# Kernel tuning notes

Measured on AMD Instinct MI355X. Metric: run time of the kernel, lower is better.

Reference implementation:

```python
import jax, jax.numpy as jnp
import numpy as np

NUM_HEADS = 16
BLOCK_SIZE = 64
NUM_GLOBAL_TOKENS = 64
WINDOW_SIZE = 256
NUM_RANDOM_BLOCKS = 3
BATCH = 2
SEQ_LEN = 4096
EMBED_DIM = 1024


def _alibi_slopes(n):
    # power-of-2 head count path of _compute_alibi_slopes
    base = 2.0 ** (-(2.0 ** (-(np.log2(n) - 3.0))))
    return jnp.asarray([base ** i for i in range(1, n + 1)], dtype=jnp.float32)


def _build_block_indices():
    nb = SEQ_LEN // BLOCK_SIZE
    ngb = NUM_GLOBAL_TOKENS // BLOCK_SIZE
    wb = WINDOW_SIZE // BLOCK_SIZE
    mb = 2 * wb + 1 + NUM_RANDOM_BLOCKS
    rng = np.random.default_rng(0)
    out = np.full((nb, mb), -1, dtype=np.int64)
    for qb in range(nb):
        attended = set(range(ngb))  # global blocks handled separately
        idx = 0
        for kb in range(max(ngb, qb - wb), min(nb, qb + wb + 1)):
            if kb not in attended:
                out[qb, idx] = kb
                attended.add(kb)
                idx += 1
        cand = [b for b in range(ngb, nb) if b not in attended]
        pick = rng.choice(len(cand), size=min(NUM_RANDOM_BLOCKS, len(cand)), replace=False)
        for j in pick:
            out[qb, idx] = cand[j]
            idx += 1
    return jnp.asarray(out)


def setup_inputs() -> dict:
    key = jax.random.key(0)
    ks = jax.random.split(key, 5)
    s = 0.02
    x = jax.random.normal(ks[0], (BATCH, SEQ_LEN, EMBED_DIM), jnp.float32)
    Wq = jax.random.normal(ks[1], (EMBED_DIM, EMBED_DIM), jnp.float32) * s
    Wk = jax.random.normal(ks[2], (EMBED_DIM, EMBED_DIM), jnp.float32) * s
    Wv = jax.random.normal(ks[3], (EMBED_DIM, EMBED_DIM), jnp.float32) * s
    Wo = jax.random.normal(ks[4], (EMBED_DIM, EMBED_DIM), jnp.float32) * s
    return {"x": x, "Wq": Wq, "Wk": Wk, "Wv": Wv, "Wo": Wo,
            "block_indices": _build_block_indices()}


def reference(x, Wq, Wk, Wv, Wo, block_indices):
    B, S, E = x.shape
    H = NUM_HEADS
    Dh = E // H
    G = NUM_GLOBAL_TOKENS
    BS = BLOCK_SIZE
    scale = 1.0 / np.sqrt(Dh)

    def split_heads(t):
        return t.reshape(B, S, H, Dh).transpose(0, 2, 1, 3)  # [B,H,S,Dh]

    q = split_heads(x @ Wq)
    k = split_heads(x @ Wk)
    v = split_heads(x @ Wv)

    slopes = _alibi_slopes(H)  # [H]
    pos = jnp.arange(S, dtype=jnp.float32)

    # ---- global tokens: full attention over all keys ----
    sg = jnp.einsum('bhgd,bhsd->bhgs', q[:, :, :G], k) * scale
    bias_g = -slopes[:, None, None] * jnp.abs(pos[:G, None] - pos[None, :])  # [H,G,S]
    pg = jax.nn.softmax(sg + bias_g[None], axis=-1)
    out_g = jnp.einsum('bhgs,bhsd->bhgd', pg, v)  # [B,H,G,Dh]

    # ---- sparse queries: global KV + gathered sparse blocks ----
    nb = S // BS
    ngb = G // BS
    nqb = nb - ngb
    bi = block_indices[ngb:]           # [nqb, MB], -1 = padding
    mb = bi.shape[1]
    bsafe = jnp.maximum(bi, 0)

    kb = k.reshape(B, H, nb, BS, Dh)
    vb = v.reshape(B, H, nb, BS, Dh)
    kg = kb[:, :, bsafe].reshape(B, H, nqb, mb * BS, Dh)
    vg = vb[:, :, bsafe].reshape(B, H, nqb, mb * BS, Dh)
    kglob = jnp.broadcast_to(k[:, :, None, :G], (B, H, nqb, G, Dh))
    vglob = jnp.broadcast_to(v[:, :, None, :G], (B, H, nqb, G, Dh))
    kcat = jnp.concatenate([kglob, kg], axis=3)  # [B,H,nqb,G+mb*BS,Dh]
    vcat = jnp.concatenate([vglob, vg], axis=3)

    qn = q[:, :, G:].reshape(B, H, nqb, BS, Dh)
    scores = jnp.einsum('bhqmd,bhqnd->bhqmn', qn, kcat) * scale

    qpos = (G + jnp.arange(nqb * BS, dtype=jnp.float32)).reshape(nqb, BS)
    loc_pos = (bsafe[:, :, None] * BS + jnp.arange(BS)[None, None, :]).reshape(nqb, mb * BS).astype(jnp.float32)
    kpos = jnp.concatenate([jnp.broadcast_to(pos[:G][None], (nqb, G)), loc_pos], axis=1)
    bias = -slopes[:, None, None, None] * jnp.abs(qpos[None, :, :, None] - kpos[None, :, None, :])  # [H,nqb,BS,Kt]

    valid = jnp.concatenate([jnp.ones((nqb, G), bool), jnp.repeat(bi >= 0, BS, axis=1)], axis=1)
    scores = jnp.where(valid[None, None, :, None, :], scores + bias[None], -jnp.inf)
    p = jax.nn.softmax(scores, axis=-1)
    out_s = jnp.einsum('bhqmn,bhqnd->bhqmd', p, vcat).reshape(B, H, S - G, Dh)

    out = jnp.concatenate([out_g, out_s], axis=2)  # [B,H,S,Dh]
    out = out.transpose(0, 2, 1, 3).reshape(B, S, E)
    return out @ Wo
```

## Files before the change

kernel.cpp:

```cpp
#include <hip/hip_runtime.h>
#include <stdint.h>

typedef __attribute__((ext_vector_type(8))) short short8;
typedef __attribute__((ext_vector_type(4))) float f32x4;
typedef __attribute__((ext_vector_type(8))) unsigned short u16x8;

#define DEV static __device__ __forceinline__

DEV unsigned short f2bf(float f) {
  union { float f; uint32_t u; } v; v.f = f;
  uint32_t r = v.u + 0x7FFFu + ((v.u >> 16) & 1u);
  return (unsigned short)(r >> 16);
}

DEV void gload16(const void* g, void* l) {
  __builtin_amdgcn_global_load_lds(
      (const __attribute__((address_space(1))) void*)g,
      (__attribute__((address_space(3))) void*)l, 16, 0, 0);
}

__global__ void cast_x_kernel(const float* __restrict__ x, unsigned short* __restrict__ xb) {
  int i = blockIdx.x * 256 + threadIdx.x;
  f32x4 a = ((const f32x4*)x)[2 * i];
  f32x4 b = ((const f32x4*)x)[2 * i + 1];
  u16x8 o;
  o[0] = f2bf(a[0]); o[1] = f2bf(a[1]); o[2] = f2bf(a[2]); o[3] = f2bf(a[3]);
  o[4] = f2bf(b[0]); o[5] = f2bf(b[1]); o[6] = f2bf(b[2]); o[7] = f2bf(b[3]);
  ((u16x8*)xb)[i] = o;
}

__global__ void transpose_w_kernel(const float* __restrict__ Wq, const float* __restrict__ Wk,
                                   const float* __restrict__ Wv, const float* __restrict__ Wo,
                                   unsigned short* __restrict__ wt) {
  __shared__ float tile[64][65];
  int z = blockIdx.z;
  const float* W = (z == 0) ? Wq : (z == 1) ? Wk : (z == 2) ? Wv : Wo;
  unsigned short* dst = wt + (size_t)z * 1024 * 1024;
  int bn = blockIdx.x, bk = blockIdx.y;
  int t = threadIdx.x;
  int c = t & 63, rr = t >> 6;
#pragma unroll
  for (int p = 0; p < 16; ++p) {
    int r = p * 4 + rr;
    tile[r][c] = W[(size_t)(bk * 64 + r) * 1024 + bn * 64 + c];
  }
  __syncthreads();
#pragma unroll
  for (int p = 0; p < 16; ++p) {
    int r2 = p * 4 + rr;
    dst[(size_t)(bn * 64 + r2) * 1024 + bk * 64 + c] = f2bf(tile[c][r2]);
  }
}

template <int MODE>
__global__ __launch_bounds__(256, 2) void gemm_bt(const unsigned short* __restrict__ A,
                                                  const unsigned short* __restrict__ Bt,
                                                  void* __restrict__ dst, float escale) {
  constexpr int K = 1024;
  __shared__ __align__(16) unsigned short As[128 * 64];
  __shared__ __align__(16) unsigned short Bs[128 * 64];
  int bn = blockIdx.x, bm = blockIdx.y;
  int tid = threadIdx.x, lane = tid & 63, w = tid >> 6;
  int wr = w >> 1, wc = w & 1;
  f32x4 acc[4][4] = {};

  int sr[4], soff[4];
#pragma unroll
  for (int i = 0; i < 4; ++i) {
    int ci = w * 4 + i;
    int r = ci * 8 + (lane >> 3);
    int cc = lane & 7;
    int scc = cc ^ (r & 7);
    sr[i] = r;
    soff[i] = scc * 8;
  }
  const unsigned short* Arow = A + (size_t)(bm * 128) * K;
  const unsigned short* Brow = Bt + (size_t)(bn * 128) * K;

  for (int k0 = 0; k0 < K; k0 += 64) {
#pragma unroll
    for (int i = 0; i < 4; ++i) {
      gload16(Arow + (size_t)sr[i] * K + k0 + soff[i], As + (w * 4 + i) * 512);
      gload16(Brow + (size_t)sr[i] * K + k0 + soff[i], Bs + (w * 4 + i) * 512);
    }
    __syncthreads();
    short8 af[2][4], bfr[2][4];
#pragma unroll
    for (int c = 0; c < 2; ++c) {
#pragma unroll
      for (int m = 0; m < 4; ++m) {
        int cc = (lane >> 4) + 4 * c;
        int ra = wr * 64 + m * 16 + (lane & 15);
        af[c][m] = *(const short8*)(As + ra * 64 + ((cc ^ (ra & 7)) * 8));
        int rb = wc * 64 + m * 16 + (lane & 15);
        bfr[c][m] = *(const short8*)(Bs + rb * 64 + ((cc ^ (rb & 7)) * 8));
      }
    }
#pragma unroll
    for (int c = 0; c < 2; ++c)
#pragma unroll
      for (int m = 0; m < 4; ++m)
#pragma unroll
        for (int n = 0; n < 4; ++n)
          acc[m][n] = __builtin_amdgcn_mfma_f32_16x16x32_bf16(af[c][m], bfr[c][n], acc[m][n], 0, 0, 0);
    __syncthreads();
  }

  int rbase = bm * 128 + wr * 64;
  int cbase = bn * 128 + wc * 64;
#pragma unroll
  for (int m = 0; m < 4; ++m)
#pragma unroll
    for (int n = 0; n < 4; ++n) {
      int row0 = rbase + m * 16 + (lane >> 4) * 4;
      int col = cbase + n * 16 + (lane & 15);
#pragma unroll
      for (int reg = 0; reg < 4; ++reg) {
        int row = row0 + reg;
        float v = acc[m][n][reg] * escale;
        if (MODE == 0) {
          ((float*)dst)[(size_t)row * 1024 + col] = v;
        } else {
          int b = row >> 12, s = row & 4095;
          int h = col >> 6, d = col & 63;
          if (MODE == 1)
            ((unsigned short*)dst)[((size_t)(b * 16 + h) * 4096 + s) * 64 + d] = f2bf(v);
          else
            ((unsigned short*)dst)[(((size_t)(b * 16 + h) * 64 + (s >> 6)) * 64 + d) * 64 + (s & 63)] = f2bf(v);
        }
      }
    }
}

__global__ __launch_bounds__(256) void attn_kernel(const unsigned short* __restrict__ Qh,
                            const unsigned short* __restrict__ Kh,
                            const unsigned short* __restrict__ Vbt,
                            const int* __restrict__ bidx,
                            unsigned short* __restrict__ attn_out,
                            float* __restrict__ Opart,
                            float* __restrict__ lpart) {
  __shared__ __align__(16) unsigned short Ks[2][64 * 64];
  __shared__ __align__(16) unsigned short Vs[2][64 * 64];
  __shared__ __align__(16) unsigned short Pl[4][16][72];
  int flat = blockIdx.x + 71 * blockIdx.y;
  int nf = (flat & 7) * 284 + (flat >> 3);
  int gx = nf % 71, bh = nf / 71;
  int h = bh & 15;
  int tid = threadIdx.x, lane = tid & 63, w = tid >> 6;
  float slope2 = exp2f(-0.5f * (float)(h + 1)) * 1.44269504f;

  int qb, nkb;
  int list[13];
  if (gx < 63) {
    qb = gx + 1;
    nkb = 1;
    list[0] = 0;
#pragma unroll
    for (int j = 0; j < 12; ++j) {
      int v = bidx[qb * 12 + j];
      if (v >= 0) list[nkb++] = v;
    }
  } else {
    qb = 0;
    int chunk = gx - 63;
    nkb = 8;
#pragma unroll
    for (int i = 0; i < 8; ++i) list[i] = chunk * 8 + i;
  }

  int qrow = qb * 64 + w * 16 + (lane & 15);
  const unsigned short* qptr = Qh + ((size_t)bh * 4096 + qrow) * 64 + (lane >> 4) * 8;
  short8 qf0 = *(const short8*)qptr;
  short8 qf1 = *(const short8*)(qptr + 32);

  float psum[4] = {0.f, 0.f, 0.f, 0.f};
  f32x4 accO[4] = {};
  int qpos0 = qb * 64 + w * 16 + (lane >> 4) * 4;

  const unsigned short* Kbh = Kh + (size_t)bh * 4096 * 64;
  const unsigned short* Vbh = Vbt + (size_t)bh * 4096 * 64;

  int sr[2], so[2];
#pragma unroll
  for (int i = 0; i < 2; ++i) {
    int ci = w * 2 + i;
    int r = ci * 8 + (lane >> 3);
    sr[i] = r;
    so[i] = ((lane & 7) ^ (r & 7)) * 8;
  }
  auto STAGE = [&](int bi, int kb) {
    const unsigned short* kbase = Kbh + (size_t)kb * 4096;
    const unsigned short* vbase = Vbh + (size_t)kb * 4096;
#pragma unroll
    for (int i = 0; i < 2; ++i) {
      gload16(kbase + sr[i] * 64 + so[i], &Ks[bi][(w * 2 + i) * 512]);
      gload16(vbase + sr[i] * 64 + so[i], &Vs[bi][(w * 2 + i) * 512]);
    }
  };

  STAGE(0, list[0]);

  for (int it = 0; it < nkb; ++it) {
    int cur = it & 1;
    int kb = list[it];
    __syncthreads();
    if (it + 1 < nkb) STAGE(cur ^ 1, list[it + 1]);

    float pv[4][4];
#pragma unroll
    for (int ct = 0; ct < 4; ++ct) {
      int kr = ct * 16 + (lane & 15);
      short8 kf0 = *(const short8*)(&Ks[cur][kr * 64 + (((lane >> 4) ^ (kr & 7)) * 8)]);
      short8 kf1 = *(const short8*)(&Ks[cur][kr * 64 + ((((lane >> 4) + 4) ^ (kr & 7)) * 8)]);
      f32x4 s = __builtin_amdgcn_mfma_f32_16x16x32_bf16(qf0, kf0, (f32x4){0.f, 0.f, 0.f, 0.f}, 0, 0, 0);
      s = __builtin_amdgcn_mfma_f32_16x16x32_bf16(qf1, kf1, s, 0, 0, 0);
      int kpos = kb * 64 + ct * 16 + (lane & 15);
#pragma unroll
      for (int reg = 0; reg < 4; ++reg) {
        float dp = fabsf((float)(qpos0 + reg - kpos));
        float p = exp2f(__builtin_fmaf(-slope2, dp, s[reg]));
        pv[ct][reg] = p;
        psum[reg] += p;
      }
    }
#pragma unroll
    for (int cp = 0; cp < 2; ++cp)
#pragma unroll
      for (int reg = 0; reg < 4; ++reg) {
        uint32_t pk;
        asm("v_cvt_pk_bf16_f32 %0, %1, %2" : "=v"(pk) : "v"(pv[2 * cp][reg]), "v"(pv[2 * cp + 1][reg]));
        int row = (lane >> 4) * 4 + reg;
        int c = lane & 15;
        Pl[w][row][cp * 32 + c] = (unsigned short)pk;
        Pl[w][row][cp * 32 + 16 + c] = (unsigned short)(pk >> 16);
      }

    asm volatile("s_waitcnt lgkmcnt(0)" ::: "memory");
    short8 pa0 = *(const short8*)(&Pl[w][lane & 15][(lane >> 4) * 8]);
    short8 pa1 = *(const short8*)(&Pl[w][lane & 15][(lane >> 4) * 8 + 32]);
#pragma unroll
    for (int dt = 0; dt < 4; ++dt) {
      int dr = dt * 16 + (lane & 15);
      short8 vf0 = *(const short8*)(&Vs[cur][dr * 64 + (((lane >> 4) ^ (dr & 7)) * 8)]);
      short8 vf1 = *(const short8*)(&Vs[cur][dr * 64 + ((((lane >> 4) + 4) ^ (dr & 7)) * 8)]);
      accO[dt] = __builtin_amdgcn_mfma_f32_16x16x32_bf16(pa0, vf0, accO[dt], 0, 0, 0);
      accO[dt] = __builtin_amdgcn_mfma_f32_16x16x32_bf16(pa1, vf1, accO[dt], 0, 0, 0);
    }
    asm volatile("s_waitcnt lgkmcnt(0)" ::: "memory");
  }

  float l[4];
#pragma unroll
  for (int reg = 0; reg < 4; ++reg) {
    float v = psum[reg];
#pragma unroll
    for (int off = 1; off < 16; off <<= 1) v += __shfl_xor(v, off, 64);
    l[reg] = v;
  }

  int b = bh >> 4;
  if (gx < 63) {
#pragma unroll
    for (int reg = 0; reg < 4; ++reg) {
      float rl = 1.0f / l[reg];
#pragma unroll
      for (int dt = 0; dt < 4; ++dt) {
        int row = qb * 64 + w * 16 + (lane >> 4) * 4 + reg;
        int col = h * 64 + dt * 16 + (lane & 15);
        attn_out[((size_t)b * 4096 + row) * 1024 + col] = f2bf(accO[dt][reg] * rl);
      }
    }
  } else {
    int chunk = gx - 63;
    float* Op = Opart + (size_t)(bh * 8 + chunk) * 64 * 64;
    float* lp = lpart + (size_t)(bh * 8 + chunk) * 64;
#pragma unroll
    for (int reg = 0; reg < 4; ++reg) {
      int row = w * 16 + (lane >> 4) * 4 + reg;
#pragma unroll
      for (int dt = 0; dt < 4; ++dt) {
        int col = dt * 16 + (lane & 15);
        Op[row * 64 + col] = accO[dt][reg];
      }
      if ((lane & 15) == 0) lp[row] = l[reg];
    }
  }
}

__global__ void merge_qb0(const float* __restrict__ Opart, const float* __restrict__ lpart,
                          unsigned short* __restrict__ attn_out) {
  int bh = blockIdx.x;
  int tid = threadIdx.x;
  int row = tid >> 2, cg = tid & 3;
  const float* lp = lpart + (size_t)bh * 8 * 64;
  float L = 0.f;
#pragma unroll
  for (int c = 0; c < 8; ++c) L += lp[c * 64 + row];
  float rL = 1.0f / L;
  int b = bh >> 4, h = bh & 15;
  f32x4 acc0 = {}, acc1 = {}, acc2 = {}, acc3 = {};
#pragma unroll
  for (int c = 0; c < 8; ++c) {
    const float* Op = Opart + ((size_t)(bh * 8 + c) * 64 + row) * 64 + cg * 16;
    acc0 += ((const f32x4*)Op)[0];
    acc1 += ((const f32x4*)Op)[1];
    acc2 += ((const f32x4*)Op)[2];
    acc3 += ((const f32x4*)Op)[3];
  }
  unsigned short* out = attn_out + ((size_t)b * 4096 + row) * 1024 + h * 64 + cg * 16;
#pragma unroll
  for (int j = 0; j < 4; ++j) {
    out[j] = f2bf(acc0[j] * rL);
    out[4 + j] = f2bf(acc1[j] * rL);
    out[8 + j] = f2bf(acc2[j] * rL);
    out[12 + j] = f2bf(acc3[j] * rL);
  }
}

extern "C" void kernel_launch(void* const* d_in, const int* in_sizes, int n_in,
                              void* d_out, int out_size, void* d_ws, size_t ws_size,
                              hipStream_t stream) {
  const float* x = (const float*)d_in[0];
  const float* Wq = (const float*)d_in[1];
  const float* Wk = (const float*)d_in[2];
  const float* Wv = (const float*)d_in[3];
  const float* Wo = (const float*)d_in[4];
  const int* bidx = (const int*)d_in[5];

  char* ws = (char*)d_ws;
  unsigned short* xb = (unsigned short*)(ws);
  unsigned short* wt = (unsigned short*)(ws + 16777216);
  unsigned short* Qb = (unsigned short*)(ws + 25165824);
  unsigned short* Kb = (unsigned short*)(ws + 41943040);
  unsigned short* Vtb = (unsigned short*)(ws + 58720256);
  unsigned short* attnb = (unsigned short*)(ws + 75497472);
  float* Opart = (float*)(ws);
  float* lpart = (float*)(ws + 4194304);

  cast_x_kernel<<<4096, 256, 0, stream>>>(x, xb);
  transpose_w_kernel<<<dim3(16, 16, 4), 256, 0, stream>>>(Wq, Wk, Wv, Wo, wt);
  gemm_bt<1><<<dim3(8, 64), 256, 0, stream>>>(xb, wt, Qb, 0.18033688f);
  gemm_bt<1><<<dim3(8, 64), 256, 0, stream>>>(xb, wt + 1048576, Kb, 1.0f);
  gemm_bt<2><<<dim3(8, 64), 256, 0, stream>>>(xb, wt + 2097152, Vtb, 1.0f);
  attn_kernel<<<dim3(71, 32), 256, 0, stream>>>(Qb, Kb, Vtb, bidx, attnb, Opart, lpart);
  merge_qb0<<<32, 256, 0, stream>>>(Opart, lpart, attnb);
  gemm_bt<0><<<dim3(8, 64), 256, 0, stream>>>(attnb, wt + 3145728, (float*)d_out, 1.0f);
}
```

Measured before the change: 196.2 us.

## Fuse QKV projections into one GEMM launch and streamline attention bias math

Merges the three Q/K/V projection GEMMs into a single 24x64-block launch, so the GPU gets more concurrent blocks and two launches go away. In attention, the ALiBi bias for off-diagonal key blocks is computed from precomputed per-row and per-column terms with no abs, since the sign of the distance is known. Adds s_setprio around the MFMA sections and double-buffers the P scratch tile so the trailing lgkmcnt wait can be dropped. The extra branches and doubled LDS for P may raise register and LDS pressure.

Result: faster. 189.9 us (-3.2%).

```diff
diff --git a/kernel.cpp b/kernel.cpp
--- a/kernel.cpp
+++ b/kernel.cpp
@@ -52,10 +52,88 @@
   }
 }
 
-template <int MODE>
-__global__ __launch_bounds__(256, 2) void gemm_bt(const unsigned short* __restrict__ A,
-                                                  const unsigned short* __restrict__ Bt,
-                                                  void* __restrict__ dst, float escale) {
+__global__ __launch_bounds__(256, 2) void gemm_qkv(const unsigned short* __restrict__ A,
+                                                   const unsigned short* __restrict__ wt,
+                                                   unsigned short* __restrict__ Qb,
+                                                   unsigned short* __restrict__ Kb,
+                                                   unsigned short* __restrict__ Vtb,
+                                                   float qscale) {
+  constexpr int K = 1024;
+  __shared__ __align__(16) unsigned short As[128 * 64];
+  __shared__ __align__(16) unsigned short Bs[128 * 64];
+  int bn = blockIdx.x, bm = blockIdx.y;
+  int which = bn >> 3, bnn = bn & 7;
+  int tid = threadIdx.x, lane = tid & 63, w = tid >> 6;
+  int wr = w >> 1, wc = w & 1;
+  f32x4 acc[4][4] = {};
+
+  int sr[4], soff[4];
+#pragma unroll
+  for (int i = 0; i < 4; ++i) {
+    int ci = w * 4 + i;
+    int r = ci * 8 + (lane >> 3);
+    sr[i] = r;
+    soff[i] = ((lane & 7) ^ (r & 7)) * 8;
+  }
+  const unsigned short* Arow = A + (size_t)(bm * 128) * K;
+  const unsigned short* Brow = wt + (size_t)which * 1048576 + (size_t)(bnn * 128) * K;
+
+  for (int k0 = 0; k0 < K; k0 += 64) {
+#pragma unroll
+    for (int i = 0; i < 4; ++i) {
+      gload16(Arow + (size_t)sr[i] * K + k0 + soff[i], As + (w * 4 + i) * 512);
+      gload16(Brow + (size_t)sr[i] * K + k0 + soff[i], Bs + (w * 4 + i) * 512);
+    }
+    __syncthreads();
+    short8 af[2][4], bfr[2][4];
+#pragma unroll
+    for (int c = 0; c < 2; ++c) {
+#pragma unroll
+      for (int m = 0; m < 4; ++m) {
+        int cc = (lane >> 4) + 4 * c;
+        int ra = wr * 64 + m * 16 + (lane & 15);
+        af[c][m] = *(const short8*)(As + ra * 64 + ((cc ^ (ra & 7)) * 8));
+        int rb = wc * 64 + m * 16 + (lane & 15);
+        bfr[c][m] = *(const short8*)(Bs + rb * 64 + ((cc ^ (rb & 7)) * 8));
+      }
+    }
+#pragma unroll
+    for (int c = 0; c < 2; ++c)
+#pragma unroll
+      for (int m = 0; m < 4; ++m)
+#pragma unroll
+        for (int n = 0; n < 4; ++n)
+          acc[m][n] = __builtin_amdgcn_mfma_f32_16x16x32_bf16(af[c][m], bfr[c][n], acc[m][n], 0, 0, 0);
+    __syncthreads();
+  }
+
+  int rbase = bm * 128 + wr * 64;
+  int cbase = bnn * 128 + wc * 64;
+#pragma unroll
+  for (int m = 0; m < 4; ++m)
+#pragma unroll
+    for (int n = 0; n < 4; ++n) {
+      int row0 = rbase + m * 16 + (lane >> 4) * 4;
+      int col = cbase + n * 16 + (lane & 15);
+      int h = col >> 6, d = col & 63;
+#pragma unroll
+      for (int reg = 0; reg < 4; ++reg) {
+        int row = row0 + reg;
+        float v = acc[m][n][reg];
+        int b = row >> 12, s = row & 4095;
+        if (which == 0)
+          Qb[((size_t)(b * 16 + h) * 4096 + s) * 64 + d] = f2bf(v * qscale);
+        else if (which == 1)
+          Kb[((size_t)(b * 16 + h) * 4096 + s) * 64 + d] = f2bf(v);
+        else
+          Vtb[(((size_t)(b * 16 + h) * 64 + (s >> 6)) * 64 + d) * 64 + (s & 63)] = f2bf(v);
+      }
+    }
+}
+
+__global__ __launch_bounds__(256, 2) void gemm_out(const unsigned short* __restrict__ A,
+                                                   const unsigned short* __restrict__ Bt,
+                                                   float* __restrict__ dst) {
   constexpr int K = 1024;
   __shared__ __align__(16) unsigned short As[128 * 64];
   __shared__ __align__(16) unsigned short Bs[128 * 64];
@@ -69,10 +147,8 @@
   for (int i = 0; i < 4; ++i) {
     int ci = w * 4 + i;
     int r = ci * 8 + (lane >> 3);
-    int cc = lane & 7;
-    int scc = cc ^ (r & 7);
     sr[i] = r;
-    soff[i] = scc * 8;
+    soff[i] = ((lane & 7) ^ (r & 7)) * 8;
   }
   const unsigned short* Arow = A + (size_t)(bm * 128) * K;
   const unsigned short* Brow = Bt + (size_t)(bn * 128) * K;
@@ -115,20 +191,8 @@
       int row0 = rbase + m * 16 + (lane >> 4) * 4;
       int col = cbase + n * 16 + (lane & 15);
 #pragma unroll
-      for (int reg = 0; reg < 4; ++reg) {
-        int row = row0 + reg;
-        float v = acc[m][n][reg] * escale;
-        if (MODE == 0) {
-          ((float*)dst)[(size_t)row * 1024 + col] = v;
-        } else {
-          int b = row >> 12, s = row & 4095;
-          int h = col >> 6, d = col & 63;
-          if (MODE == 1)
-            ((unsigned short*)dst)[((size_t)(b * 16 + h) * 4096 + s) * 64 + d] = f2bf(v);
-          else
-            ((unsigned short*)dst)[(((size_t)(b * 16 + h) * 64 + (s >> 6)) * 64 + d) * 64 + (s & 63)] = f2bf(v);
-        }
-      }
+      for (int reg = 0; reg < 4; ++reg)
+        dst[(size_t)(row0 + reg) * 1024 + col] = acc[m][n][reg];
     }
 }
 
@@ -141,7 +205,7 @@
                             float* __restrict__ lpart) {
   __shared__ __align__(16) unsigned short Ks[2][64 * 64];
   __shared__ __align__(16) unsigned short Vs[2][64 * 64];
-  __shared__ __align__(16) unsigned short Pl[4][16][72];
+  __shared__ __align__(16) unsigned short Pl[2][4][16][72];
   int flat = blockIdx.x + 71 * blockIdx.y;
   int nf = (flat & 7) * 284 + (flat >> 3);
   int gx = nf % 71, bh = nf / 71;
@@ -177,6 +241,16 @@
   f32x4 accO[4] = {};
   int qpos0 = qb * 64 + w * 16 + (lane >> 4) * 4;
 
+  float qposf[4], fm[4], fp[4], kctf[4];
+#pragma unroll
+  for (int reg = 0; reg < 4; ++reg) {
+    qposf[reg] = (float)(qpos0 + reg);
+    fm[reg] = -slope2 * qposf[reg];
+    fp[reg] = slope2 * qposf[reg];
+  }
+#pragma unroll
+  for (int ct = 0; ct < 4; ++ct) kctf[ct] = (float)(ct * 16 + (lane & 15));
+
   const unsigned short* Kbh = Kh + (size_t)bh * 4096 * 64;
   const unsigned short* Vbh = Vbt + (size_t)bh * 4096 * 64;
 
@@ -206,23 +280,66 @@
     __syncthreads();
     if (it + 1 < nkb) STAGE(cur ^ 1, list[it + 1]);
 
+    float kbf = (float)(kb * 64);
+    float skb = slope2 * kbf;
     float pv[4][4];
-#pragma unroll
-    for (int ct = 0; ct < 4; ++ct) {
-      int kr = ct * 16 + (lane & 15);
-      short8 kf0 = *(const short8*)(&Ks[cur][kr * 64 + (((lane >> 4) ^ (kr & 7)) * 8)]);
-      short8 kf1 = *(const short8*)(&Ks[cur][kr * 64 + ((((lane >> 4) + 4) ^ (kr & 7)) * 8)]);
-      f32x4 s = __builtin_amdgcn_mfma_f32_16x16x32_bf16(qf0, kf0, (f32x4){0.f, 0.f, 0.f, 0.f}, 0, 0, 0);
-      s = __builtin_amdgcn_mfma_f32_16x16x32_bf16(qf1, kf1, s, 0, 0, 0);
-      int kpos = kb * 64 + ct * 16 + (lane & 15);
-#pragma unroll
-      for (int reg = 0; reg < 4; ++reg) {
-        float dp = fabsf((float)(qpos0 + reg - kpos));
-        float p = exp2f(__builtin_fmaf(-slope2, dp, s[reg]));
-        pv[ct][reg] = p;
-        psum[reg] += p;
-      }
-    }
+
+    if (kb != qb) {
+      float d_[4][4];
+      if (kb < qb) {
+#pragma unroll
+        for (int ct = 0; ct < 4; ++ct) {
+          float e = __builtin_fmaf(slope2, kctf[ct], skb);
+#pragma unroll
+          for (int reg = 0; reg < 4; ++reg) d_[ct][reg] = fm[reg] + e;
+        }
+      } else {
+#pragma unroll
+        for (int ct = 0; ct < 4; ++ct) {
+          float e = __builtin_fmaf(slope2, kctf[ct], skb);
+#pragma unroll
+          for (int reg = 0; reg < 4; ++reg) d_[ct][reg] = fp[reg] - e;
+        }
+      }
+      __builtin_amdgcn_s_setprio(1);
+#pragma unroll
+      for (int ct = 0; ct < 4; ++ct) {
+        int kr = ct * 16 + (lane & 15);
+        short8 kf0 = *(const short8*)(&Ks[cur][kr * 64 + (((lane >> 4) ^ (kr & 7)) * 8)]);
+        short8 kf1 = *(const short8*)(&Ks[cur][kr * 64 + ((((lane >> 4) + 4) ^ (kr & 7)) * 8)]);
+        f32x4 s = __builtin_amdgcn_mfma_f32_16x16x32_bf16(qf0, kf0, (f32x4){0.f, 0.f, 0.f, 0.f}, 0, 0, 0);
+        s = __builtin_amdgcn_mfma_f32_16x16x32_bf16(qf1, kf1, s, 0, 0, 0);
+#pragma unroll
+        for (int reg = 0; reg < 4; ++reg) {
+          float p = exp2f(s[reg] + d_[ct][reg]);
+          pv[ct][reg] = p;
+          psum[reg] += p;
+        }
+      }
+      __builtin_amdgcn_s_setprio(0);
+    } else {
+      float qmb[4];
+#pragma unroll
+      for (int reg = 0; reg < 4; ++reg) qmb[reg] = qposf[reg] - kbf;
+      __builtin_amdgcn_s_setprio(1);
+#pragma unroll
+      for (int ct = 0; ct < 4; ++ct) {
+        int kr = ct * 16 + (lane & 15);
+        short8 kf0 = *(const short8*)(&Ks[cur][kr * 64 + (((lane >> 4) ^ (kr & 7)) * 8)]);
+        short8 kf1 = *(const short8*)(&Ks[cur][kr * 64 + ((((lane >> 4) + 4) ^ (kr & 7)) * 8)]);
+        f32x4 s = __builtin_amdgcn_mfma_f32_16x16x32_bf16(qf0, kf0, (f32x4){0.f, 0.f, 0.f, 0.f}, 0, 0, 0);
+        s = __builtin_amdgcn_mfma_f32_16x16x32_bf16(qf1, kf1, s, 0, 0, 0);
+#pragma unroll
+        for (int reg = 0; reg < 4; ++reg) {
+          float diff = qmb[reg] - kctf[ct];
+          float p = exp2f(__builtin_fmaf(-slope2, fabsf(diff), s[reg]));
+          pv[ct][reg] = p;
+          psum[reg] += p;
+        }
+      }
+      __builtin_amdgcn_s_setprio(0);
+    }
+
 #pragma unroll
     for (int cp = 0; cp < 2; ++cp)
 #pragma unroll
@@ -231,13 +348,14 @@
         asm("v_cvt_pk_bf16_f32 %0, %1, %2" : "=v"(pk) : "v"(pv[2 * cp][reg]), "v"(pv[2 * cp + 1][reg]));
         int row = (lane >> 4) * 4 + reg;
         int c = lane & 15;
-        Pl[w][row][cp * 32 + c] = (unsigned short)pk;
-        Pl[w][row][cp * 32 + 16 + c] = (unsigned short)(pk >> 16);
+        Pl[cur][w][row][cp * 32 + c] = (unsigned short)pk;
+        Pl[cur][w][row][cp * 32 + 16 + c] = (unsigned short)(pk >> 16);
       }
 
     asm volatile("s_waitcnt lgkmcnt(0)" ::: "memory");
-    short8 pa0 = *(const short8*)(&Pl[w][lane & 15][(lane >> 4) * 8]);
-    short8 pa1 = *(const short8*)(&Pl[w][lane & 15][(lane >> 4) * 8 + 32]);
+    short8 pa0 = *(const short8*)(&Pl[cur][w][lane & 15][(lane >> 4) * 8]);
+    short8 pa1 = *(const short8*)(&Pl[cur][w][lane & 15][(lane >> 4) * 8 + 32]);
+    __builtin_amdgcn_s_setprio(1);
 #pragma unroll
     for (int dt = 0; dt < 4; ++dt) {
       int dr = dt * 16 + (lane & 15);
@@ -246,7 +364,7 @@
       accO[dt] = __builtin_amdgcn_mfma_f32_16x16x32_bf16(pa0, vf0, accO[dt], 0, 0, 0);
       accO[dt] = __builtin_amdgcn_mfma_f32_16x16x32_bf16(pa1, vf1, accO[dt], 0, 0, 0);
     }
-    asm volatile("s_waitcnt lgkmcnt(0)" ::: "memory");
+    __builtin_amdgcn_s_setprio(0);
   }
 
   float l[4];
@@ -339,10 +457,8 @@
 
   cast_x_kernel<<<4096, 256, 0, stream>>>(x, xb);
   transpose_w_kernel<<<dim3(16, 16, 4), 256, 0, stream>>>(Wq, Wk, Wv, Wo, wt);
-  gemm_bt<1><<<dim3(8, 64), 256, 0, stream>>>(xb, wt, Qb, 0.18033688f);
-  gemm_bt<1><<<dim3(8, 64), 256, 0, stream>>>(xb, wt + 1048576, Kb, 1.0f);
-  gemm_bt<2><<<dim3(8, 64), 256, 0, stream>>>(xb, wt + 2097152, Vtb, 1.0f);
+  gemm_qkv<<<dim3(24, 64), 256, 0, stream>>>(xb, wt, Qb, Kb, Vtb, 0.18033688f);
   attn_kernel<<<dim3(71, 32), 256, 0, stream>>>(Qb, Kb, Vtb, bidx, attnb, Opart, lpart);
   merge_qb0<<<32, 256, 0, stream>>>(Opart, lpart, attnb);
-  gemm_bt<0><<<dim3(8, 64), 256, 0, stream>>>(attnb, wt + 3145728, (float*)d_out, 1.0f);
-}
+  gemm_out<<<dim3(8, 64), 256, 0, stream>>>(attnb, wt + 3145728, (float*)d_out);
+}
```
